# Kernel optimization log

Hardware: AMD Instinct MI355X
Metric: run time of the kernel (lower is better)

## Reference

```python
import jax, jax.numpy as jnp
import numpy as np

B, S, D, H = 2, 2048, 1024, 16

def setup_inputs() -> dict:
    key = jax.random.key(0)
    ks = jax.random.split(key, 5)
    s = 0.02
    return {
        "x": jax.random.normal(ks[0], (B, S, D), dtype=jnp.float32),
        "Wq": jax.random.normal(ks[1], (D, D), dtype=jnp.float32) * s,
        "bq": jnp.zeros((D,), dtype=jnp.float32),
        "Wk": jax.random.normal(ks[2], (D, D), dtype=jnp.float32) * s,
        "bk": jnp.zeros((D,), dtype=jnp.float32),
        "Wv": jax.random.normal(ks[3], (D, D), dtype=jnp.float32) * s,
        "bv": jnp.zeros((D,), dtype=jnp.float32),
        "Wp": jax.random.normal(ks[4], (D, D), dtype=jnp.float32) * s,
        "bp": jnp.zeros((D,), dtype=jnp.float32),
    }

def reference(x, Wq, bq, Wk, bk, Wv, bv, Wp, bp):
    b, s, d = x.shape
    hd = d // H
    # QKV projections, split into heads: [b, H, s, hd]
    q = (x @ Wq.T + bq).reshape(b, s, H, hd).transpose(0, 2, 1, 3)
    k = (x @ Wk.T + bk).reshape(b, s, H, hd).transpose(0, 2, 1, 3)
    v = (x @ Wv.T + bv).reshape(b, s, H, hd).transpose(0, 2, 1, 3)
    # NOTE: original scales by 1/sqrt(embedding_size), not head_dim
    att = jnp.einsum("bhqd,bhkd->bhqk", q, k) / jnp.sqrt(jnp.float32(d))
    causal = jnp.tril(jnp.ones((s, s), dtype=bool))
    att = jnp.where(causal[None, None], att, -jnp.inf)
    att = jax.nn.softmax(att, axis=-1)
    y = jnp.einsum("bhqk,bhkd->bhqd", att, v)
    y = y.transpose(0, 2, 1, 3).reshape(b, s, d)
    return y @ Wp.T + bp
```

## Files before the change

### kernel.cpp

```cpp
#include <hip/hip_runtime.h>
#include <hip/hip_bf16.h>

#define B_  2
#define S_  2048
#define D_  1024
#define H_  16
#define HD_ 64

typedef float  f32x4 __attribute__((ext_vector_type(4)));
typedef __bf16 bf16x8 __attribute__((ext_vector_type(8)));

__device__ __forceinline__ unsigned short f2bf(float f) {
    __bf16 h = (__bf16)f;
    return __builtin_bit_cast(unsigned short, h);
}

__device__ __forceinline__ void gload_lds16(const unsigned short* g, unsigned short* l) {
    __builtin_amdgcn_global_load_lds(
        (const __attribute__((address_space(1))) unsigned int*)g,
        (__attribute__((address_space(3))) unsigned int*)l, 16, 0, 0);
}

__global__ __launch_bounds__(256) void cvt5(
    const float* __restrict__ x,  const float* __restrict__ wq,
    const float* __restrict__ wk, const float* __restrict__ wv,
    const float* __restrict__ wp,
    unsigned short* __restrict__ xb, unsigned short* __restrict__ wqkv,
    unsigned short* __restrict__ wpb)
{
    const int bid = blockIdx.x;
    const float* src; unsigned short* dst; int off;
    if (bid < 4096)      { src = x;  dst = xb;              off = bid * 1024; }
    else if (bid < 5120) { src = wq; dst = wqkv;            off = (bid - 4096) * 1024; }
    else if (bid < 6144) { src = wk; dst = wqkv + (1<<20);  off = (bid - 5120) * 1024; }
    else if (bid < 7168) { src = wv; dst = wqkv + (2<<20);  off = (bid - 6144) * 1024; }
    else                 { src = wp; dst = wpb;             off = (bid - 7168) * 1024; }
    const int i = off + threadIdx.x * 4;
    float4 v = *reinterpret_cast<const float4*>(src + i);
    ushort4 o;
    o.x = f2bf(v.x); o.y = f2bf(v.y); o.z = f2bf(v.z); o.w = f2bf(v.w);
    *reinterpret_cast<ushort4*>(dst + i) = o;
}

template <int MODE>
__global__ __launch_bounds__(256, 2) void gemm128(
    const unsigned short* __restrict__ A,
    const unsigned short* __restrict__ Bm,
    const float* __restrict__ bias,
    void* __restrict__ C0, void* __restrict__ C1, void* __restrict__ C2,
    int M, int N, int K)
{
    __shared__ unsigned short As[128 * 64];
    __shared__ unsigned short Bs[128 * 64];
    const int tid  = threadIdx.x;
    const int lane = tid & 63;
    const int w    = tid >> 6;
    const int wm   = w >> 1, wn = w & 1;
    const int m0   = blockIdx.x << 7, n0 = blockIdx.y << 7;
    const int l15  = lane & 15, l4 = lane >> 4;
    const int r8   = lane >> 3;
    const int c8   = (lane & 7) << 3;

    f32x4 acc[4][4] = {};

    for (int k0 = 0; k0 < K; k0 += 64) {
        if (k0) __syncthreads();
        #pragma unroll
        for (int i = 0; i < 4; ++i) {
            const int row = i * 32 + w * 8;
            gload_lds16(A  + (size_t)(m0 + row + r8) * K + k0 + c8, As + row * 64);
            gload_lds16(Bm + (size_t)(n0 + row + r8) * K + k0 + c8, Bs + row * 64);
        }
        __syncthreads();
        #pragma unroll
        for (int kk = 0; kk < 2; ++kk) {
            bf16x8 af[4], bf[4];
            #pragma unroll
            for (int mi = 0; mi < 4; ++mi)
                af[mi] = *reinterpret_cast<const bf16x8*>(&As[(wm * 64 + mi * 16 + l15) * 64 + kk * 32 + l4 * 8]);
            #pragma unroll
            for (int ni = 0; ni < 4; ++ni)
                bf[ni] = *reinterpret_cast<const bf16x8*>(&Bs[(wn * 64 + ni * 16 + l15) * 64 + kk * 32 + l4 * 8]);
            #pragma unroll
            for (int mi = 0; mi < 4; ++mi)
                #pragma unroll
                for (int ni = 0; ni < 4; ++ni)
                    acc[mi][ni] = __builtin_amdgcn_mfma_f32_16x16x32_bf16(af[mi], bf[ni], acc[mi][ni], 0, 0, 0);
        }
    }

    #pragma unroll
    for (int mi = 0; mi < 4; ++mi) {
        #pragma unroll
        for (int ni = 0; ni < 4; ++ni) {
            const int colg = n0 + wn * 64 + ni * 16 + l15;
            const float bv = bias[colg];
            const int rowb = m0 + wm * 64 + mi * 16 + l4 * 4;
            if constexpr (MODE == 0) {
                float* C = (float*)C0;
                #pragma unroll
                for (int j = 0; j < 4; ++j)
                    C[(size_t)(rowb + j) * N + colg] = acc[mi][ni][j] + bv;
            } else {
                const int region = n0 >> 10;
                const int cl = colg & 1023;
                if (region < 2) {
                    unsigned short* C = (unsigned short*)(region ? C1 : C0);
                    #pragma unroll
                    for (int j = 0; j < 4; ++j)
                        C[(size_t)(rowb + j) * 1024 + cl] = f2bf(acc[mi][ni][j] + bv);
                } else {
                    ushort4 pk;
                    pk.x = f2bf(acc[mi][ni][0] + bv);
                    pk.y = f2bf(acc[mi][ni][1] + bv);
                    pk.z = f2bf(acc[mi][ni][2] + bv);
                    pk.w = f2bf(acc[mi][ni][3] + bv);
                    const int bb = rowb >> 11, s = rowb & (S_ - 1);
                    unsigned short* vt = (unsigned short*)C2 +
                        ((size_t)(bb * H_ + (cl >> 6)) * HD_ + (cl & 63)) * S_ + s;
                    *reinterpret_cast<ushort4*>(vt) = pk;
                }
            }
        }
    }
}

#define SC_ 0.04508422f
__global__ __launch_bounds__(64, 2) void attn6(
    const unsigned short* __restrict__ qb,
    const unsigned short* __restrict__ kb,
    const unsigned short* __restrict__ vt,
    unsigned short* __restrict__ yb)
{
    __shared__ unsigned short Plds[32][88];

    const int lane = threadIdx.x;
    const int l15  = lane & 15, l4 = lane >> 4;

    const int bid  = blockIdx.x;
    const int xcd  = bid & 7;
    const int idx  = bid >> 3;
    const int hb   = xcd * 4 + (idx >> 6);
    const int qi   = 63 - (idx & 63);
    const int h    = hb & 15, b = hb >> 4;

    const int q0w  = qi * 32;
    const size_t baseTok = (size_t)b * S_;
    const unsigned short* kgh = kb + baseTok * D_ + h * HD_;
    const unsigned short* vth = vt + (size_t)(b * H_ + h) * HD_ * S_;

    bf16x8 qf[2][2];
    #pragma unroll
    for (int m = 0; m < 2; ++m)
        #pragma unroll
        for (int kh = 0; kh < 2; ++kh)
            qf[m][kh] = *reinterpret_cast<const bf16x8*>(
                qb + (baseTok + q0w + m * 16 + l15) * D_ + h * HD_ + kh * 32 + l4 * 8);

    f32x4 o_acc[2][4] = {};
    float l_part[2][4] = {};

    const int nkv = (q0w + 95) >> 6;

    bf16x8 kf[4][2];
    #pragma unroll
    for (int kvb = 0; kvb < 4; ++kvb)
        #pragma unroll
        for (int kh = 0; kh < 2; ++kh)
            kf[kvb][kh] = *reinterpret_cast<const bf16x8*>(
                kgh + (size_t)(kvb * 16 + l15) * D_ + kh * 32 + l4 * 8);

    for (int t = 0; t < nkv; ++t) {
        const int kv0 = t << 6;
        const bool last = (t == nkv - 1);

        f32x4 s0[4] = {}, s1[4] = {};
        __builtin_amdgcn_s_setprio(1);
        #pragma unroll
        for (int kvb = 0; kvb < 4; ++kvb)
            #pragma unroll
            for (int kh = 0; kh < 2; ++kh)
                s0[kvb] = __builtin_amdgcn_mfma_f32_16x16x32_bf16(
                    qf[0][kh], kf[kvb][kh], s0[kvb], 0, 0, 0);
        #pragma unroll
        for (int kvb = 0; kvb < 4; ++kvb)
            #pragma unroll
            for (int kh = 0; kh < 2; ++kh)
                s1[kvb] = __builtin_amdgcn_mfma_f32_16x16x32_bf16(
                    qf[1][kh], kf[kvb][kh], s1[kvb], 0, 0, 0);
        __builtin_amdgcn_s_setprio(0);

        if (t + 1 < nkv) {
            #pragma unroll
            for (int kvb = 0; kvb < 4; ++kvb)
                #pragma unroll
                for (int kh = 0; kh < 2; ++kh)
                    kf[kvb][kh] = *reinterpret_cast<const bf16x8*>(
                        kgh + (size_t)(kv0 + 64 + kvb * 16 + l15) * D_ + kh * 32 + l4 * 8);
        }

        bf16x8 vf0[4];
        #pragma unroll
        for (int nb = 0; nb < 4; ++nb)
            vf0[nb] = *reinterpret_cast<const bf16x8*>(
                vth + (size_t)(nb * 16 + l15) * S_ + kv0 + l4 * 8);

        const int r = l4 * 4;
        if (!last) {
            #pragma unroll
            for (int j = 0; j < 4; ++j) {
                float p0 = exp2f(s0[0][j] * SC_), p1 = exp2f(s0[1][j] * SC_);
                float p2 = exp2f(s0[2][j] * SC_), p3 = exp2f(s0[3][j] * SC_);
                l_part[0][j] += (p0 + p1) + (p2 + p3);
                Plds[r + j][l15]      = f2bf(p0);
                Plds[r + j][16 + l15] = f2bf(p1);
                Plds[r + j][32 + l15] = f2bf(p2);
                Plds[r + j][48 + l15] = f2bf(p3);
            }
            #pragma unroll
            for (int j = 0; j < 4; ++j) {
                float p0 = exp2f(s1[0][j] * SC_), p1 = exp2f(s1[1][j] * SC_);
                float p2 = exp2f(s1[2][j] * SC_), p3 = exp2f(s1[3][j] * SC_);
                l_part[1][j] += (p0 + p1) + (p2 + p3);
                Plds[16 + r + j][l15]      = f2bf(p0);
                Plds[16 + r + j][16 + l15] = f2bf(p1);
                Plds[16 + r + j][32 + l15] = f2bf(p2);
                Plds[16 + r + j][48 + l15] = f2bf(p3);
            }
        } else {
            #pragma unroll
            for (int j = 0; j < 4; ++j) {
                const int rowg = q0w + r + j;
                float p[4];
                #pragma unroll
                for (int kvb = 0; kvb < 4; ++kvb) {
                    const bool ok = (kv0 + kvb * 16 + l15 <= rowg);
                    p[kvb] = ok ? exp2f(s0[kvb][j] * SC_) : 0.f;
                    Plds[r + j][kvb * 16 + l15] = f2bf(p[kvb]);
                }
                l_part[0][j] += (p[0] + p[1]) + (p[2] + p[3]);
            }
            #pragma unroll
            for (int j = 0; j < 4; ++j) {
                const int rowg = q0w + 16 + r + j;
                float p[4];
                #pragma unroll
                for (int kvb = 0; kvb < 4; ++kvb) {
                    const bool ok = (kv0 + kvb * 16 + l15 <= rowg);
                    p[kvb] = ok ? exp2f(s1[kvb][j] * SC_) : 0.f;
                    Plds[16 + r + j][kvb * 16 + l15] = f2bf(p[kvb]);
                }
                l_part[1][j] += (p[0] + p[1]) + (p[2] + p[3]);
            }
        }

        bf16x8 vf1[4];
        #pragma unroll
        for (int nb = 0; nb < 4; ++nb)
            vf1[nb] = *reinterpret_cast<const bf16x8*>(
                vth + (size_t)(nb * 16 + l15) * S_ + kv0 + 32 + l4 * 8);

        {
            bf16x8 pf0 = *reinterpret_cast<const bf16x8*>(&Plds[l15][l4 * 8]);
            bf16x8 pf1 = *reinterpret_cast<const bf16x8*>(&Plds[16 + l15][l4 * 8]);
            __builtin_amdgcn_s_setprio(1);
            #pragma unroll
            for (int nb = 0; nb < 4; ++nb) {
                o_acc[0][nb] = __builtin_amdgcn_mfma_f32_16x16x32_bf16(pf0, vf0[nb], o_acc[0][nb], 0, 0, 0);
                o_acc[1][nb] = __builtin_amdgcn_mfma_f32_16x16x32_bf16(pf1, vf0[nb], o_acc[1][nb], 0, 0, 0);
            }
            __builtin_amdgcn_s_setprio(0);
        }
        {
            bf16x8 pf0 = *reinterpret_cast<const bf16x8*>(&Plds[l15][32 + l4 * 8]);
            bf16x8 pf1 = *reinterpret_cast<const bf16x8*>(&Plds[16 + l15][32 + l4 * 8]);
            __builtin_amdgcn_s_setprio(1);
            #pragma unroll
            for (int nb = 0; nb < 4; ++nb) {
                o_acc[0][nb] = __builtin_amdgcn_mfma_f32_16x16x32_bf16(pf0, vf1[nb], o_acc[0][nb], 0, 0, 0);
                o_acc[1][nb] = __builtin_amdgcn_mfma_f32_16x16x32_bf16(pf1, vf1[nb], o_acc[1][nb], 0, 0, 0);
            }
            __builtin_amdgcn_s_setprio(0);
        }
    }

    float l[8];
    #pragma unroll
    for (int m = 0; m < 2; ++m)
        #pragma unroll
        for (int j = 0; j < 4; ++j)
            l[m * 4 + j] = l_part[m][j];
    #pragma unroll
    for (int st = 1; st <= 8; st <<= 1) {
        float tv[8];
        #pragma unroll
        for (int i = 0; i < 8; ++i) tv[i] = __shfl_xor(l[i], st);
        #pragma unroll
        for (int i = 0; i < 8; ++i) l[i] += tv[i];
    }
    #pragma unroll
    for (int m = 0; m < 2; ++m) {
        #pragma unroll
        for (int j = 0; j < 4; ++j) {
            const float inv = 1.0f / l[m * 4 + j];
            const int rowg = q0w + m * 16 + l4 * 4 + j;
            unsigned short* yp = yb + (baseTok + rowg) * D_ + h * HD_ + l15;
            #pragma unroll
            for (int nb = 0; nb < 4; ++nb)
                yp[nb * 16] = f2bf(o_acc[m][nb][j] * inv);
        }
    }
}

extern "C" void kernel_launch(void* const* d_in, const int* in_sizes, int n_in,
                              void* d_out, int out_size, void* d_ws, size_t ws_size,
                              hipStream_t stream)
{
    const float* x  = (const float*)d_in[0];
    const float* Wq = (const float*)d_in[1];
    const float* bq = (const float*)d_in[2];
    const float* Wk = (const float*)d_in[3];
    const float* bk = (const float*)d_in[4];
    const float* Wv = (const float*)d_in[5];
    const float* bv = (const float*)d_in[6];
    const float* Wp = (const float*)d_in[7];
    const float* bp = (const float*)d_in[8];

    char* ws = (char*)d_ws;
    const size_t MB = 1024 * 1024;
    unsigned short* xb    = (unsigned short*)(ws);
    unsigned short* wqkvb = (unsigned short*)(ws + 8 * MB);
    unsigned short* wpb   = (unsigned short*)(ws + 14 * MB);
    unsigned short* qbuf  = (unsigned short*)(ws + 16 * MB);
    unsigned short* kbuf  = (unsigned short*)(ws + 24 * MB);
    unsigned short* vtbf  = (unsigned short*)(ws + 32 * MB);
    unsigned short* ybuf  = (unsigned short*)(ws + 40 * MB);
    float*          bcat  = (float*)(ws + 48 * MB);

    const int M = B_ * S_;

    cvt5<<<8192, 256, 0, stream>>>(x, Wq, Wk, Wv, Wp, xb, wqkvb, wpb);
    hipMemcpyAsync(bcat,          bq, D_ * sizeof(float), hipMemcpyDeviceToDevice, stream);
    hipMemcpyAsync(bcat + D_,     bk, D_ * sizeof(float), hipMemcpyDeviceToDevice, stream);
    hipMemcpyAsync(bcat + 2 * D_, bv, D_ * sizeof(float), hipMemcpyDeviceToDevice, stream);

    gemm128<1><<<dim3(M / 128, 3072 / 128, 1), 256, 0, stream>>>(
        xb, wqkvb, bcat, qbuf, kbuf, vtbf, M, 3072, D_);

    attn6<<<2048, 64, 0, stream>>>(qbuf, kbuf, vtbf, ybuf);

    gemm128<0><<<dim3(M / 128, D_ / 128, 1), 256, 0, stream>>>(
        ybuf, wpb, bp, (float*)d_out, nullptr, nullptr, M, D_, D_);
}
```

Baseline: 248.5 us.

## Split GEMM kernels, use 64-row proj tiles, and interleave causal attention block order

The templated GEMM is split into two kernels. The QKV GEMM gets a launch bound of 3 blocks per SM. The output projection becomes a 64x128 tile kernel, doubling its grid from 256 to 512 blocks so more CUs are busy. The attention block order now alternates heavy and light causal query tiles within each group, to even out load across concurrently scheduled blocks. The occupancy hint may force register spills in the QKV GEMM, and the smaller projection tiles reduce data reuse.

```diff
diff --git a/kernel.cpp b/kernel.cpp
--- a/kernel.cpp
+++ b/kernel.cpp
@@ -42,8 +42,7 @@
     *reinterpret_cast<ushort4*>(dst + i) = o;
 }
 
-template <int MODE>
-__global__ __launch_bounds__(256, 2) void gemm128(
+__global__ __launch_bounds__(256, 3) void gemm128_qkv(
     const unsigned short* __restrict__ A,
     const unsigned short* __restrict__ Bm,
     const float* __restrict__ bias,
@@ -89,6 +88,7 @@
         }
     }
 
+    const int region = n0 >> 10;
     #pragma unroll
     for (int mi = 0; mi < 4; ++mi) {
         #pragma unroll
@@ -96,37 +96,90 @@
             const int colg = n0 + wn * 64 + ni * 16 + l15;
             const float bv = bias[colg];
             const int rowb = m0 + wm * 64 + mi * 16 + l4 * 4;
-            if constexpr (MODE == 0) {
-                float* C = (float*)C0;
+            const int cl = colg & 1023;
+            if (region < 2) {
+                unsigned short* C = (unsigned short*)(region ? C1 : C0);
                 #pragma unroll
                 for (int j = 0; j < 4; ++j)
-                    C[(size_t)(rowb + j) * N + colg] = acc[mi][ni][j] + bv;
+                    C[(size_t)(rowb + j) * 1024 + cl] = f2bf(acc[mi][ni][j] + bv);
             } else {
-                const int region = n0 >> 10;
-                const int cl = colg & 1023;
-                if (region < 2) {
-                    unsigned short* C = (unsigned short*)(region ? C1 : C0);
-                    #pragma unroll
-                    for (int j = 0; j < 4; ++j)
-                        C[(size_t)(rowb + j) * 1024 + cl] = f2bf(acc[mi][ni][j] + bv);
-                } else {
-                    ushort4 pk;
-                    pk.x = f2bf(acc[mi][ni][0] + bv);
-                    pk.y = f2bf(acc[mi][ni][1] + bv);
-                    pk.z = f2bf(acc[mi][ni][2] + bv);
-                    pk.w = f2bf(acc[mi][ni][3] + bv);
-                    const int bb = rowb >> 11, s = rowb & (S_ - 1);
-                    unsigned short* vt = (unsigned short*)C2 +
-                        ((size_t)(bb * H_ + (cl >> 6)) * HD_ + (cl & 63)) * S_ + s;
-                    *reinterpret_cast<ushort4*>(vt) = pk;
-                }
-            }
+                ushort4 pk;
+                pk.x = f2bf(acc[mi][ni][0] + bv);
+                pk.y = f2bf(acc[mi][ni][1] + bv);
+                pk.z = f2bf(acc[mi][ni][2] + bv);
+                pk.w = f2bf(acc[mi][ni][3] + bv);
+                const int bb = rowb >> 11, s = rowb & (S_ - 1);
+                unsigned short* vt = (unsigned short*)C2 +
+                    ((size_t)(bb * H_ + (cl >> 6)) * HD_ + (cl & 63)) * S_ + s;
+                *reinterpret_cast<ushort4*>(vt) = pk;
+            }
+        }
+    }
+}
+
+__global__ __launch_bounds__(256, 2) void gemm64_proj(
+    const unsigned short* __restrict__ A,
+    const unsigned short* __restrict__ Bm,
+    const float* __restrict__ bias,
+    float* __restrict__ C,
+    int M, int N, int K)
+{
+    __shared__ unsigned short As[64 * 64];
+    __shared__ unsigned short Bs[128 * 64];
+    const int tid  = threadIdx.x;
+    const int lane = tid & 63;
+    const int w    = tid >> 6;
+    const int m0   = blockIdx.x << 6, n0 = blockIdx.y << 7;
+    const int l15  = lane & 15, l4 = lane >> 4;
+    const int r8   = lane >> 3;
+    const int c8   = (lane & 7) << 3;
+
+    f32x4 acc[4][2] = {};
+
+    for (int k0 = 0; k0 < K; k0 += 64) {
+        if (k0) __syncthreads();
+        #pragma unroll
+        for (int i = 0; i < 6; ++i) {
+            const int c = w * 6 + i;
+            if (c < 8)
+                gload_lds16(A  + (size_t)(m0 + c * 8 + r8) * K + k0 + c8, As + c * 512);
+            else
+                gload_lds16(Bm + (size_t)(n0 + (c - 8) * 8 + r8) * K + k0 + c8, Bs + (c - 8) * 512);
+        }
+        __syncthreads();
+        #pragma unroll
+        for (int kk = 0; kk < 2; ++kk) {
+            bf16x8 af[4], bf[2];
+            #pragma unroll
+            for (int mi = 0; mi < 4; ++mi)
+                af[mi] = *reinterpret_cast<const bf16x8*>(&As[(mi * 16 + l15) * 64 + kk * 32 + l4 * 8]);
+            #pragma unroll
+            for (int ni = 0; ni < 2; ++ni)
+                bf[ni] = *reinterpret_cast<const bf16x8*>(&Bs[(w * 32 + ni * 16 + l15) * 64 + kk * 32 + l4 * 8]);
+            #pragma unroll
+            for (int mi = 0; mi < 4; ++mi)
+                #pragma unroll
+                for (int ni = 0; ni < 2; ++ni)
+                    acc[mi][ni] = __builtin_amdgcn_mfma_f32_16x16x32_bf16(af[mi], bf[ni], acc[mi][ni], 0, 0, 0);
+        }
+    }
+
+    #pragma unroll
+    for (int mi = 0; mi < 4; ++mi) {
+        #pragma unroll
+        for (int ni = 0; ni < 2; ++ni) {
+            const int colg = n0 + w * 32 + ni * 16 + l15;
+            const float bv = bias[colg];
+            const int rowb = m0 + mi * 16 + l4 * 4;
+            #pragma unroll
+            for (int j = 0; j < 4; ++j)
+                C[(size_t)(rowb + j) * N + colg] = acc[mi][ni][j] + bv;
         }
     }
 }
 
 #define SC_ 0.04508422f
-__global__ __launch_bounds__(64, 2) void attn6(
+__global__ __launch_bounds__(64, 2) void attn7(
     const unsigned short* __restrict__ qb,
     const unsigned short* __restrict__ kb,
     const unsigned short* __restrict__ vt,
@@ -141,7 +194,8 @@
     const int xcd  = bid & 7;
     const int idx  = bid >> 3;
     const int hb   = xcd * 4 + (idx >> 6);
-    const int qi   = 63 - (idx & 63);
+    const int j32  = idx & 31;
+    const int qi   = ((idx >> 5) & 1) ? j32 : 63 - j32;
     const int h    = hb & 15, b = hb >> 4;
 
     const int q0w  = qi * 32;
@@ -344,11 +398,11 @@
     hipMemcpyAsync(bcat + D_,     bk, D_ * sizeof(float), hipMemcpyDeviceToDevice, stream);
     hipMemcpyAsync(bcat + 2 * D_, bv, D_ * sizeof(float), hipMemcpyDeviceToDevice, stream);
 
-    gemm128<1><<<dim3(M / 128, 3072 / 128, 1), 256, 0, stream>>>(
+    gemm128_qkv<<<dim3(M / 128, 3072 / 128, 1), 256, 0, stream>>>(
         xb, wqkvb, bcat, qbuf, kbuf, vtbf, M, 3072, D_);
 
-    attn6<<<2048, 64, 0, stream>>>(qbuf, kbuf, vtbf, ybuf);
-
-    gemm128<0><<<dim3(M / 128, D_ / 128, 1), 256, 0, stream>>>(
-        ybuf, wpb, bp, (float*)d_out, nullptr, nullptr, M, D_, D_);
-}
+    attn7<<<2048, 64, 0, stream>>>(qbuf, kbuf, vtbf, ybuf);
+
+    gemm64_proj<<<dim3(M / 64, D_ / 128, 1), 256, 0, stream>>>(
+        ybuf, wpb, bp, (float*)d_out, M, D_, D_);
+}
```

Result: faster. 219.3 us (-11.8%).
